# Kernel tuning notes

Measured on AMD Instinct MI355X. Metric: run time of the kernel, lower is better.

The kernel has to match this reference:

```python
import jax, jax.numpy as jnp
import numpy as np

N_HEADS = 16
WINDOW = 256
GLOBAL_IDX = np.array([0])

def _global_local_mask(seq_len):
    # allowed[i,j] = True if |i-j|<=window OR i is global OR j is global
    i = jnp.arange(seq_len)[:, None]
    j = jnp.arange(seq_len)[None, :]
    g = jnp.asarray(GLOBAL_IDX)
    row_global = jnp.isin(jnp.arange(seq_len), g)
    allowed = (jnp.abs(i - j) <= WINDOW) | row_global[:, None] | row_global[None, :]
    return allowed

def setup_inputs() -> dict:
    key = jax.random.key(0)
    ks = jax.random.split(key, 9)
    B, S, D = 1, 2048, 1024
    w = 0.02
    return {
        "x": jax.random.normal(ks[0], (B, S, D), jnp.float32),
        "Wq": jax.random.normal(ks[1], (D, D), jnp.float32) * w,
        "bq": jnp.zeros((D,), jnp.float32),
        "Wk": jax.random.normal(ks[2], (D, D), jnp.float32) * w,
        "bk": jnp.zeros((D,), jnp.float32),
        "Wv": jax.random.normal(ks[3], (D, D), jnp.float32) * w,
        "bv": jnp.zeros((D,), jnp.float32),
        "Wo": jax.random.normal(ks[4], (D, D), jnp.float32) * w,
        "bo": jnp.zeros((D,), jnp.float32),
    }

def reference(x, Wq, bq, Wk, bk, Wv, bv, Wo, bo):
    B, S, D = x.shape
    H = N_HEADS
    Dh = D // H
    scale = Dh ** -0.5
    # projections (torch Linear: y = x @ W^T + b; here W stored as [in,out] equivalent)
    q = (x @ Wq + bq).reshape(B, S, H, Dh)
    k = (x @ Wk + bk).reshape(B, S, H, Dh)
    v = (x @ Wv + bv).reshape(B, S, H, Dh)
    # dense scores [B,H,S,S]
    scores = jnp.einsum("bqhd,bkhd->bhqk", q, k) * scale
    allowed = _global_local_mask(S)  # [S,S] bool
    scores = jnp.where(allowed[None, None], scores, -jnp.inf)
    attn = jax.nn.softmax(scores, axis=-1)
    out = jnp.einsum("bhqk,bkhd->bqhd", attn, v).reshape(B, S, D)
    return out @ Wo + bo
```

## Files before the change

### kernel.cpp

```cpp
#include <hip/hip_runtime.h>
#include <hip/hip_bf16.h>
#include <math.h>

#define S_LEN   2048
#define DM      1024
#define NH      16
#define DH      64
#define WIN     256

typedef __attribute__((ext_vector_type(8))) short          bf16x8;
typedef __attribute__((ext_vector_type(4))) float          f32x4;
typedef __attribute__((ext_vector_type(8))) unsigned short u16x8;
typedef __attribute__((ext_vector_type(4))) unsigned short u16x4;
typedef unsigned short u16;

#define GLDS(gsrc, ldst)                                                        \
    __builtin_amdgcn_global_load_lds(                                           \
        (const __attribute__((address_space(1))) void*)(gsrc),                  \
        (__attribute__((address_space(3))) void*)(ldst), 16, 0, 0)

__device__ __forceinline__ u16 f2bf(float f) {
    union { float f; unsigned u; } v; v.f = f;
    unsigned r = v.u + 0x7FFF + ((v.u >> 16) & 1);
    return (u16)(r >> 16);
}

__global__ __launch_bounds__(256) void cvt_x_kernel(const float* __restrict__ x,
                                                    u16* __restrict__ xb) {
    int i = (blockIdx.x * 256 + threadIdx.x) * 8;
    float4 a = *(const float4*)&x[i];
    float4 b = *(const float4*)&x[i + 4];
    u16x8 o;
    o[0] = f2bf(a.x); o[1] = f2bf(a.y); o[2] = f2bf(a.z); o[3] = f2bf(a.w);
    o[4] = f2bf(b.x); o[5] = f2bf(b.y); o[6] = f2bf(b.z); o[7] = f2bf(b.w);
    *(u16x8*)&xb[i] = o;
}

__global__ __launch_bounds__(256) void cvt_wT_kernel(const float* __restrict__ Wq,
                                                     const float* __restrict__ Wk,
                                                     const float* __restrict__ Wv,
                                                     const float* __restrict__ Wo,
                                                     u16* __restrict__ WT) {
    __shared__ float Ws[64][65];
    const float* W = (blockIdx.z == 0) ? Wq : (blockIdx.z == 1) ? Wk
                   : (blockIdx.z == 2) ? Wv : Wo;
    u16* dst = WT + (size_t)blockIdx.z * (1u << 20);
    const int k0 = blockIdx.x * 64, n0 = blockIdx.y * 64;
    const int tid = threadIdx.x;
#pragma unroll
    for (int p = 0; p < 4; ++p) {
        int flat = tid + p * 256;
        int row = flat >> 4, c4 = (flat & 15) * 4;
        float4 v = *(const float4*)&W[(k0 + row) * DM + n0 + c4];
        Ws[row][c4 + 0] = v.x; Ws[row][c4 + 1] = v.y;
        Ws[row][c4 + 2] = v.z; Ws[row][c4 + 3] = v.w;
    }
    __syncthreads();
#pragma unroll
    for (int p = 0; p < 4; ++p) {
        int flat = tid + p * 256;
        int n = flat >> 4, k4 = (flat & 15) * 4;
        u16x4 o;
#pragma unroll
        for (int j = 0; j < 4; ++j) o[j] = f2bf(Ws[k4 + j][n]);
        *(u16x4*)&dst[(n0 + n) * DM + k0 + k4] = o;
    }
}

template<bool OBF>
__device__ __forceinline__ void gemm_mfma_body(const u16* __restrict__ A,
                                               const u16* __restrict__ Bt,
                                               const float* __restrict__ bias,
                                               u16* __restrict__ Cb,
                                               float* __restrict__ Cf) {
    __shared__ __align__(16) u16 As[64 * 64];
    __shared__ __align__(16) u16 Bs[128 * 64];
    const int tid = threadIdx.x;
    const int l = tid & 63, w = tid >> 6;
    const int wm = w >> 1, wn = w & 1;
    const int l15 = l & 15, lh = l >> 4;
    const int brow = blockIdx.y * 64, bcol = blockIdx.x * 128;

    f32x4 acc[2][4];
#pragma unroll
    for (int i = 0; i < 2; ++i)
#pragma unroll
        for (int j = 0; j < 4; ++j) acc[i][j] = (f32x4)0.f;

    const int lr = l >> 3, lc = l & 7, g = lc ^ lr;
    const u16* aSrc = A  + (size_t)(brow + w * 16 + lr) * DM + g * 8;
    const u16* bSrc = Bt + (size_t)(bcol + w * 32 + lr) * DM + g * 8;

    for (int k0 = 0; k0 < DM; k0 += 64) {
        __syncthreads();
#pragma unroll
        for (int i = 0; i < 2; ++i)
            GLDS(aSrc + i * 8 * DM + k0, &As[(w * 2 + i) * 512]);
#pragma unroll
        for (int i = 0; i < 4; ++i)
            GLDS(bSrc + i * 8 * DM + k0, &Bs[(w * 4 + i) * 512]);
        __syncthreads();

#pragma unroll
        for (int ks = 0; ks < 2; ++ks) {
            bf16x8 af[2], bf[4];
#pragma unroll
            for (int i = 0; i < 2; ++i) {
                int ra = wm * 32 + i * 16 + l15;
                af[i] = *(const bf16x8*)&As[ra * 64 + (((ks * 4 + lh) ^ (ra & 7)) * 8)];
            }
#pragma unroll
            for (int j = 0; j < 4; ++j) {
                int rb = wn * 64 + j * 16 + l15;
                bf[j] = *(const bf16x8*)&Bs[rb * 64 + (((ks * 4 + lh) ^ (rb & 7)) * 8)];
            }
#pragma unroll
            for (int i = 0; i < 2; ++i)
#pragma unroll
                for (int j = 0; j < 4; ++j)
                    acc[i][j] = __builtin_amdgcn_mfma_f32_16x16x32_bf16(af[i], bf[j], acc[i][j], 0, 0, 0);
        }
    }
#pragma unroll
    for (int j = 0; j < 4; ++j) {
        int gcol = bcol + wn * 64 + j * 16 + l15;
        float bz = bias[gcol];
#pragma unroll
        for (int i = 0; i < 2; ++i) {
            int grow = brow + wm * 32 + i * 16 + lh * 4;
#pragma unroll
            for (int rr = 0; rr < 4; ++rr) {
                float v = acc[i][j][rr] + bz;
                if (OBF) Cb[(grow + rr) * DM + gcol] = f2bf(v);
                else     Cf[(grow + rr) * DM + gcol] = v;
            }
        }
    }
}

__global__ __launch_bounds__(256) void qkv_mfma_kernel(
        const u16* __restrict__ xb,
        const u16* __restrict__ WqT, const float* __restrict__ bq, u16* __restrict__ Qb,
        const u16* __restrict__ WkT, const float* __restrict__ bk, u16* __restrict__ Kb,
        const u16* __restrict__ WvT, const float* __restrict__ bv, u16* __restrict__ Vb) {
    const u16* Wt; const float* b; u16* C;
    if (blockIdx.z == 0)      { Wt = WqT; b = bq; C = Qb; }
    else if (blockIdx.z == 1) { Wt = WkT; b = bk; C = Kb; }
    else                      { Wt = WvT; b = bv; C = Vb; }
    gemm_mfma_body<true>(xb, Wt, b, C, nullptr);
}

__global__ __launch_bounds__(256) void oproj_mfma_kernel(
        const u16* __restrict__ Ob, const u16* __restrict__ WoT,
        const float* __restrict__ bo, float* __restrict__ out) {
    gemm_mfma_body<false>(Ob, WoT, bo, nullptr, out);
}

__global__ __launch_bounds__(256) void vT_kernel(const u16* __restrict__ Vb,
                                                 u16* __restrict__ VT) {
    const int j0 = blockIdx.x * 64, h = blockIdx.y;
    const int tid = threadIdx.x;
#pragma unroll
    for (int p = 0; p < 2; ++p) {
        int flat = tid + p * 256;
        int dh = flat >> 3, tc = flat & 7;
        u16x8 o;
#pragma unroll
        for (int t = 0; t < 8; ++t)
            o[t] = Vb[(j0 + tc * 8 + t) * DM + h * DH + dh];
        *(u16x8*)&VT[(h * DH + dh) * S_LEN + j0 + tc * 8] = o;
    }
}

__global__ __launch_bounds__(256) void attn_mfma_kernel(const u16* __restrict__ Qb,
                                                        const u16* __restrict__ Kb,
                                                        const u16* __restrict__ VT,
                                                        u16* __restrict__ Ob) {
    __shared__ __align__(16) u16 Pl[4 * 16 * 72];
    const int tid = threadIdx.x;
    const int w = tid >> 6, l = tid & 63;
    const int l15 = l & 15, lh = l >> 4;
    const int i0 = blockIdx.x * 64, h = blockIdx.y;
    const int q0 = i0 + w * 16;
    u16* Pw = &Pl[w * 16 * 72];

    bf16x8 qf[2];
    {
        int qr = q0 + l15;
        qf[0] = *(const bf16x8*)&Qb[qr * DM + h * DH + lh * 8];
        qf[1] = *(const bf16x8*)&Qb[qr * DM + h * DH + 32 + lh * 8];
    }

    f32x4 o[4];
    float ls[4] = {0.f, 0.f, 0.f, 0.f};
#pragma unroll
    for (int fc = 0; fc < 4; ++fc) o[fc] = (f32x4)0.f;

    int t_lo, t_hi;
    if (q0 == 0) { t_lo = 0; t_hi = S_LEN / 64 - 1; }
    else {
        int lo = q0 - WIN;      if (lo < 0) lo = 0;
        int hi = q0 + 15 + WIN; if (hi > S_LEN - 1) hi = S_LEN - 1;
        t_lo = lo >> 6; t_hi = hi >> 6;
    }
    const int nband = t_hi - t_lo + 1;
    const int nt = nband + (t_lo > 0 ? 1 : 0);

    bf16x8 kf[2][4];
    {
        const int j0 = t_lo << 6;
#pragma unroll
        for (int ks = 0; ks < 2; ++ks)
#pragma unroll
            for (int fc = 0; fc < 4; ++fc)
                kf[ks][fc] = *(const bf16x8*)&Kb[(j0 + fc * 16 + l15) * DM + h * DH + ks * 32 + lh * 8];
    }

    for (int it = 0; it < nt; ++it) {
        const int j0 = ((it < nband) ? (t_lo + it) : 0) << 6;

        bf16x8 vf[2][4];
#pragma unroll
        for (int ks = 0; ks < 2; ++ks)
#pragma unroll
            for (int fc = 0; fc < 4; ++fc)
                vf[ks][fc] = *(const bf16x8*)&VT[(h * DH + fc * 16 + l15) * S_LEN + j0 + ks * 32 + lh * 8];

        f32x4 s[4];
#pragma unroll
        for (int fc = 0; fc < 4; ++fc) s[fc] = (f32x4)0.f;
#pragma unroll
        for (int ks = 0; ks < 2; ++ks)
#pragma unroll
            for (int fc = 0; fc < 4; ++fc)
                s[fc] = __builtin_amdgcn_mfma_f32_16x16x32_bf16(qf[ks], kf[ks][fc], s[fc], 0, 0, 0);

        {
            const int itn = (it + 1 < nt) ? it + 1 : it;
            const int jn = ((itn < nband) ? (t_lo + itn) : 0) << 6;
            bf16x8 kn[2][4];
#pragma unroll
            for (int ks = 0; ks < 2; ++ks)
#pragma unroll
                for (int fc = 0; fc < 4; ++fc)
                    kn[ks][fc] = *(const bf16x8*)&Kb[(jn + fc * 16 + l15) * DM + h * DH + ks * 32 + lh * 8];

#pragma unroll
            for (int fc = 0; fc < 4; ++fc)
#pragma unroll
                for (int rr = 0; rr < 4; ++rr) {
                    int r = q0 + lh * 4 + rr;
                    int c = j0 + fc * 16 + l15;
                    int d = r - c;
                    bool ok = (d <= WIN && -d <= WIN) || (r == 0) || (c == 0);
                    s[fc][rr] = ok ? __expf(s[fc][rr] * 0.125f) : 0.f;
                }
#pragma unroll
            for (int rr = 0; rr < 4; ++rr)
                ls[rr] += (s[0][rr] + s[1][rr]) + (s[2][rr] + s[3][rr]);

#pragma unroll
            for (int fc = 0; fc < 4; ++fc)
#pragma unroll
                for (int rr = 0; rr < 4; ++rr)
                    Pw[(lh * 4 + rr) * 72 + fc * 16 + l15] = f2bf(s[fc][rr]);
            asm volatile("s_waitcnt lgkmcnt(0)" ::: "memory");

#pragma unroll
            for (int ks = 0; ks < 2; ++ks) {
                bf16x8 pa = *(const bf16x8*)&Pw[l15 * 72 + ks * 32 + lh * 8];
#pragma unroll
                for (int fc = 0; fc < 4; ++fc)
                    o[fc] = __builtin_amdgcn_mfma_f32_16x16x32_bf16(pa, vf[ks][fc], o[fc], 0, 0, 0);
            }

#pragma unroll
            for (int ks = 0; ks < 2; ++ks)
#pragma unroll
                for (int fc = 0; fc < 4; ++fc)
                    kf[ks][fc] = kn[ks][fc];
        }
    }

#pragma unroll
    for (int rr = 0; rr < 4; ++rr) {
#pragma unroll
        for (int mk = 1; mk < 16; mk <<= 1)
            ls[rr] += __shfl_xor(ls[rr], mk, 64);
    }

#pragma unroll
    for (int rr = 0; rr < 4; ++rr) {
        float inv = 1.0f / ls[rr];
#pragma unroll
        for (int fc = 0; fc < 4; ++fc)
            Ob[(q0 + lh * 4 + rr) * DM + h * DH + fc * 16 + l15] = f2bf(o[fc][rr] * inv);
    }
}

extern "C" void kernel_launch(void* const* d_in, const int* in_sizes, int n_in,
                              void* d_out, int out_size, void* d_ws, size_t ws_size,
                              hipStream_t stream) {
    const float* x  = (const float*)d_in[0];
    const float* Wq = (const float*)d_in[1];
    const float* bq = (const float*)d_in[2];
    const float* Wk = (const float*)d_in[3];
    const float* bk = (const float*)d_in[4];
    const float* Wv = (const float*)d_in[5];
    const float* bv = (const float*)d_in[6];
    const float* Wo = (const float*)d_in[7];
    const float* bo = (const float*)d_in[8];
    float* out = (float*)d_out;

    char* W = (char*)d_ws;
    u16* xb  = (u16*)(W);
    u16* WT  = (u16*)(W + ((size_t)4  << 20));
    u16* Qb  = (u16*)(W + ((size_t)12 << 20));
    u16* Kb  = (u16*)(W + ((size_t)16 << 20));
    u16* Vb  = (u16*)(W + ((size_t)20 << 20));
    u16* VT  = (u16*)(W + ((size_t)24 << 20));
    u16* Ob  = xb;
    const u16* WqT = WT;
    const u16* WkT = WT + (1u << 20);
    const u16* WvT = WT + (2u << 20);
    const u16* WoT = WT + (3u << 20);

    cvt_x_kernel <<<dim3(S_LEN * DM / (256 * 8)), 256, 0, stream>>>(x, xb);
    cvt_wT_kernel<<<dim3(16, 16, 4), 256, 0, stream>>>(Wq, Wk, Wv, Wo, WT);
    qkv_mfma_kernel<<<dim3(8, 32, 3), 256, 0, stream>>>(xb, WqT, bq, Qb,
                                                        WkT, bk, Kb, WvT, bv, Vb);
    vT_kernel<<<dim3(32, 16), 256, 0, stream>>>(Vb, VT);
    attn_mfma_kernel<<<dim3(32, 16), 256, 0, stream>>>(Qb, Kb, VT, Ob);
    oproj_mfma_kernel<<<dim3(8, 32), 256, 0, stream>>>(Ob, WoT, bo, out);
}
```

Before: 174.3 us.

## Fuse V transpose into QKV epilogue and split attention key range across wave pairs

The V projection now writes its output transposed straight from the GEMM epilogue, which removes the separate vT_kernel launch and its round trip through memory. The attention kernel now handles 32 queries per block, with two waves sharing each 16-query group and each taking half of the key tiles. The halves merge their partial outputs and row sums through shared memory after a block barrier. This doubles the grid and evens out the load from the long global-row tile. In exchange it adds a sync and LDS traffic, and the transposed V stores are narrow, strided 8-byte writes.

```diff
diff --git a/kernel.cpp b/kernel.cpp
--- a/kernel.cpp
+++ b/kernel.cpp
@@ -67,7 +67,7 @@
     }
 }
 
-template<bool OBF>
+template<int OMODE>
 __device__ __forceinline__ void gemm_mfma_body(const u16* __restrict__ A,
                                                const u16* __restrict__ Bt,
                                                const float* __restrict__ bias,
@@ -128,11 +128,18 @@
 #pragma unroll
         for (int i = 0; i < 2; ++i) {
             int grow = brow + wm * 32 + i * 16 + lh * 4;
-#pragma unroll
-            for (int rr = 0; rr < 4; ++rr) {
-                float v = acc[i][j][rr] + bz;
-                if (OBF) Cb[(grow + rr) * DM + gcol] = f2bf(v);
-                else     Cf[(grow + rr) * DM + gcol] = v;
+            if (OMODE == 2) {
+                u16x4 tv;
+#pragma unroll
+                for (int rr = 0; rr < 4; ++rr) tv[rr] = f2bf(acc[i][j][rr] + bz);
+                *(u16x4*)&Cb[(size_t)gcol * S_LEN + grow] = tv;
+            } else {
+#pragma unroll
+                for (int rr = 0; rr < 4; ++rr) {
+                    float v = acc[i][j][rr] + bz;
+                    if (OMODE == 0) Cb[(grow + rr) * DM + gcol] = f2bf(v);
+                    else            Cf[(grow + rr) * DM + gcol] = v;
+                }
             }
         }
     }
@@ -142,46 +149,29 @@
         const u16* __restrict__ xb,
         const u16* __restrict__ WqT, const float* __restrict__ bq, u16* __restrict__ Qb,
         const u16* __restrict__ WkT, const float* __restrict__ bk, u16* __restrict__ Kb,
-        const u16* __restrict__ WvT, const float* __restrict__ bv, u16* __restrict__ Vb) {
-    const u16* Wt; const float* b; u16* C;
-    if (blockIdx.z == 0)      { Wt = WqT; b = bq; C = Qb; }
-    else if (blockIdx.z == 1) { Wt = WkT; b = bk; C = Kb; }
-    else                      { Wt = WvT; b = bv; C = Vb; }
-    gemm_mfma_body<true>(xb, Wt, b, C, nullptr);
+        const u16* __restrict__ WvT, const float* __restrict__ bv, u16* __restrict__ VT) {
+    if (blockIdx.z == 0)      gemm_mfma_body<0>(xb, WqT, bq, Qb, nullptr);
+    else if (blockIdx.z == 1) gemm_mfma_body<0>(xb, WkT, bk, Kb, nullptr);
+    else                      gemm_mfma_body<2>(xb, WvT, bv, VT, nullptr);
 }
 
 __global__ __launch_bounds__(256) void oproj_mfma_kernel(
         const u16* __restrict__ Ob, const u16* __restrict__ WoT,
         const float* __restrict__ bo, float* __restrict__ out) {
-    gemm_mfma_body<false>(Ob, WoT, bo, nullptr, out);
-}
-
-__global__ __launch_bounds__(256) void vT_kernel(const u16* __restrict__ Vb,
-                                                 u16* __restrict__ VT) {
-    const int j0 = blockIdx.x * 64, h = blockIdx.y;
-    const int tid = threadIdx.x;
-#pragma unroll
-    for (int p = 0; p < 2; ++p) {
-        int flat = tid + p * 256;
-        int dh = flat >> 3, tc = flat & 7;
-        u16x8 o;
-#pragma unroll
-        for (int t = 0; t < 8; ++t)
-            o[t] = Vb[(j0 + tc * 8 + t) * DM + h * DH + dh];
-        *(u16x8*)&VT[(h * DH + dh) * S_LEN + j0 + tc * 8] = o;
-    }
-}
-
-__global__ __launch_bounds__(256) void attn_mfma_kernel(const u16* __restrict__ Qb,
-                                                        const u16* __restrict__ Kb,
-                                                        const u16* __restrict__ VT,
-                                                        u16* __restrict__ Ob) {
+    gemm_mfma_body<1>(Ob, WoT, bo, nullptr, out);
+}
+
+__global__ __launch_bounds__(256, 4) void attn_mfma_kernel(
+        const u16* __restrict__ Qb, const u16* __restrict__ Kb,
+        const u16* __restrict__ VT, u16* __restrict__ Ob) {
     __shared__ __align__(16) u16 Pl[4 * 16 * 72];
+    __shared__ __align__(16) float MB[2][64][20];
     const int tid = threadIdx.x;
     const int w = tid >> 6, l = tid & 63;
+    const int qg = w >> 1, half = w & 1;
     const int l15 = l & 15, lh = l >> 4;
-    const int i0 = blockIdx.x * 64, h = blockIdx.y;
-    const int q0 = i0 + w * 16;
+    const int i0 = blockIdx.x * 32, h = blockIdx.y;
+    const int q0 = i0 + qg * 16;
     u16* Pw = &Pl[w * 16 * 72];
 
     bf16x8 qf[2];
@@ -197,18 +187,20 @@
     for (int fc = 0; fc < 4; ++fc) o[fc] = (f32x4)0.f;
 
     int t_lo, t_hi;
-    if (q0 == 0) { t_lo = 0; t_hi = S_LEN / 64 - 1; }
-    else {
+    {
         int lo = q0 - WIN;      if (lo < 0) lo = 0;
         int hi = q0 + 15 + WIN; if (hi > S_LEN - 1) hi = S_LEN - 1;
+        if (q0 == 0) hi = S_LEN - 1;
         t_lo = lo >> 6; t_hi = hi >> 6;
     }
     const int nband = t_hi - t_lo + 1;
     const int nt = nband + (t_lo > 0 ? 1 : 0);
+    const int b0 = half ? ((nt + 1) >> 1) : 0;
+    const int b1 = half ? nt : ((nt + 1) >> 1);
 
     bf16x8 kf[2][4];
-    {
-        const int j0 = t_lo << 6;
+    if (b0 < b1) {
+        const int j0 = ((b0 < nband) ? (t_lo + b0) : 0) << 6;
 #pragma unroll
         for (int ks = 0; ks < 2; ++ks)
 #pragma unroll
@@ -216,7 +208,7 @@
                 kf[ks][fc] = *(const bf16x8*)&Kb[(j0 + fc * 16 + l15) * DM + h * DH + ks * 32 + lh * 8];
     }
 
-    for (int it = 0; it < nt; ++it) {
+    for (int it = b0; it < b1; ++it) {
         const int j0 = ((it < nband) ? (t_lo + it) : 0) << 6;
 
         bf16x8 vf[2][4];
@@ -235,66 +227,81 @@
             for (int fc = 0; fc < 4; ++fc)
                 s[fc] = __builtin_amdgcn_mfma_f32_16x16x32_bf16(qf[ks], kf[ks][fc], s[fc], 0, 0, 0);
 
-        {
-            const int itn = (it + 1 < nt) ? it + 1 : it;
-            const int jn = ((itn < nband) ? (t_lo + itn) : 0) << 6;
-            bf16x8 kn[2][4];
-#pragma unroll
-            for (int ks = 0; ks < 2; ++ks)
-#pragma unroll
-                for (int fc = 0; fc < 4; ++fc)
-                    kn[ks][fc] = *(const bf16x8*)&Kb[(jn + fc * 16 + l15) * DM + h * DH + ks * 32 + lh * 8];
-
-#pragma unroll
-            for (int fc = 0; fc < 4; ++fc)
-#pragma unroll
-                for (int rr = 0; rr < 4; ++rr) {
-                    int r = q0 + lh * 4 + rr;
-                    int c = j0 + fc * 16 + l15;
-                    int d = r - c;
-                    bool ok = (d <= WIN && -d <= WIN) || (r == 0) || (c == 0);
-                    s[fc][rr] = ok ? __expf(s[fc][rr] * 0.125f) : 0.f;
-                }
+        const int itn = (it + 1 < b1) ? it + 1 : it;
+        const int jn = ((itn < nband) ? (t_lo + itn) : 0) << 6;
+        bf16x8 kn[2][4];
+#pragma unroll
+        for (int ks = 0; ks < 2; ++ks)
+#pragma unroll
+            for (int fc = 0; fc < 4; ++fc)
+                kn[ks][fc] = *(const bf16x8*)&Kb[(jn + fc * 16 + l15) * DM + h * DH + ks * 32 + lh * 8];
+
+#pragma unroll
+        for (int fc = 0; fc < 4; ++fc)
+#pragma unroll
+            for (int rr = 0; rr < 4; ++rr) {
+                int r = q0 + lh * 4 + rr;
+                int c = j0 + fc * 16 + l15;
+                int d = r - c;
+                bool ok = (d <= WIN && -d <= WIN) || (r == 0) || (c == 0);
+                s[fc][rr] = ok ? __expf(s[fc][rr] * 0.125f) : 0.f;
+            }
+#pragma unroll
+        for (int rr = 0; rr < 4; ++rr)
+            ls[rr] += (s[0][rr] + s[1][rr]) + (s[2][rr] + s[3][rr]);
+
+#pragma unroll
+        for (int fc = 0; fc < 4; ++fc)
 #pragma unroll
             for (int rr = 0; rr < 4; ++rr)
-                ls[rr] += (s[0][rr] + s[1][rr]) + (s[2][rr] + s[3][rr]);
-
-#pragma unroll
-            for (int fc = 0; fc < 4; ++fc)
-#pragma unroll
-                for (int rr = 0; rr < 4; ++rr)
-                    Pw[(lh * 4 + rr) * 72 + fc * 16 + l15] = f2bf(s[fc][rr]);
-            asm volatile("s_waitcnt lgkmcnt(0)" ::: "memory");
-
-#pragma unroll
-            for (int ks = 0; ks < 2; ++ks) {
-                bf16x8 pa = *(const bf16x8*)&Pw[l15 * 72 + ks * 32 + lh * 8];
-#pragma unroll
-                for (int fc = 0; fc < 4; ++fc)
-                    o[fc] = __builtin_amdgcn_mfma_f32_16x16x32_bf16(pa, vf[ks][fc], o[fc], 0, 0, 0);
-            }
-
-#pragma unroll
-            for (int ks = 0; ks < 2; ++ks)
-#pragma unroll
-                for (int fc = 0; fc < 4; ++fc)
-                    kf[ks][fc] = kn[ks][fc];
-        }
-    }
-
-#pragma unroll
-    for (int rr = 0; rr < 4; ++rr) {
-#pragma unroll
-        for (int mk = 1; mk < 16; mk <<= 1)
-            ls[rr] += __shfl_xor(ls[rr], mk, 64);
-    }
-
-#pragma unroll
-    for (int rr = 0; rr < 4; ++rr) {
-        float inv = 1.0f / ls[rr];
+                Pw[(lh * 4 + rr) * 72 + fc * 16 + l15] = f2bf(s[fc][rr]);
+        asm volatile("s_waitcnt lgkmcnt(0)" ::: "memory");
+
+#pragma unroll
+        for (int ks = 0; ks < 2; ++ks) {
+            bf16x8 pa = *(const bf16x8*)&Pw[l15 * 72 + ks * 32 + lh * 8];
+#pragma unroll
+            for (int fc = 0; fc < 4; ++fc)
+                o[fc] = __builtin_amdgcn_mfma_f32_16x16x32_bf16(pa, vf[ks][fc], o[fc], 0, 0, 0);
+        }
+
+#pragma unroll
+        for (int ks = 0; ks < 2; ++ks)
+#pragma unroll
+            for (int fc = 0; fc < 4; ++fc)
+                kf[ks][fc] = kn[ks][fc];
+    }
+
+    if (half == 1) {
 #pragma unroll
         for (int fc = 0; fc < 4; ++fc)
-            Ob[(q0 + lh * 4 + rr) * DM + h * DH + fc * 16 + l15] = f2bf(o[fc][rr] * inv);
+            *(f32x4*)&MB[qg][l][fc * 4] = o[fc];
+        *(f32x4*)&MB[qg][l][16] = (f32x4){ls[0], ls[1], ls[2], ls[3]};
+    }
+    __syncthreads();
+    if (half == 0) {
+#pragma unroll
+        for (int fc = 0; fc < 4; ++fc) {
+            f32x4 po = *(const f32x4*)&MB[qg][l][fc * 4];
+            o[fc] += po;
+        }
+        f32x4 pl = *(const f32x4*)&MB[qg][l][16];
+#pragma unroll
+        for (int rr = 0; rr < 4; ++rr) ls[rr] += pl[rr];
+
+#pragma unroll
+        for (int rr = 0; rr < 4; ++rr)
+#pragma unroll
+            for (int mk = 1; mk < 16; mk <<= 1)
+                ls[rr] += __shfl_xor(ls[rr], mk, 64);
+
+#pragma unroll
+        for (int rr = 0; rr < 4; ++rr) {
+            float inv = 1.0f / ls[rr];
+#pragma unroll
+            for (int fc = 0; fc < 4; ++fc)
+                Ob[(q0 + lh * 4 + rr) * DM + h * DH + fc * 16 + l15] = f2bf(o[fc][rr] * inv);
+        }
     }
 }
 
@@ -317,8 +324,7 @@
     u16* WT  = (u16*)(W + ((size_t)4  << 20));
     u16* Qb  = (u16*)(W + ((size_t)12 << 20));
     u16* Kb  = (u16*)(W + ((size_t)16 << 20));
-    u16* Vb  = (u16*)(W + ((size_t)20 << 20));
-    u16* VT  = (u16*)(W + ((size_t)24 << 20));
+    u16* VT  = (u16*)(W + ((size_t)20 << 20));
     u16* Ob  = xb;
     const u16* WqT = WT;
     const u16* WkT = WT + (1u << 20);
@@ -328,8 +334,7 @@
     cvt_x_kernel <<<dim3(S_LEN * DM / (256 * 8)), 256, 0, stream>>>(x, xb);
     cvt_wT_kernel<<<dim3(16, 16, 4), 256, 0, stream>>>(Wq, Wk, Wv, Wo, WT);
     qkv_mfma_kernel<<<dim3(8, 32, 3), 256, 0, stream>>>(xb, WqT, bq, Qb,
-                                                        WkT, bk, Kb, WvT, bv, Vb);
-    vT_kernel<<<dim3(32, 16), 256, 0, stream>>>(Vb, VT);
-    attn_mfma_kernel<<<dim3(32, 16), 256, 0, stream>>>(Qb, Kb, VT, Ob);
+                                                        WkT, bk, Kb, WvT, bv, VT);
+    attn_mfma_kernel<<<dim3(64, 16), 256, 0, stream>>>(Qb, Kb, VT, Ob);
     oproj_mfma_kernel<<<dim3(8, 32), 256, 0, stream>>>(Ob, WoT, bo, out);
 }
```

New measurement: 198.3 us. +13.8%, slower.
